# Optimization experiments

Measured on AMD Instinct MI355X. Metric: run time of the kernel, lower is better.

## Reference

```python
import jax, jax.numpy as jnp
import numpy as np
from jax import lax

NPOINT = 2048
NSAMPLE = 32
RADIUS = 0.2


def setup_inputs() -> dict:
    key = jax.random.key(0)
    ks = jax.random.split(key, 6)
    B, N, C = 4, 16384, 64
    xyz = jax.random.normal(ks[0], (B, N, 3), jnp.float32)
    features = jax.random.normal(ks[1], (B, C, N), jnp.float32)

    def w(k, o, i):
        return jax.random.normal(k, (o, i), jnp.float32) * (1.0 / np.sqrt(i))

    W1 = w(ks[2], 64, C + 3)
    b1 = jnp.zeros((64,), jnp.float32)
    W2 = w(ks[3], 64, 64)
    b2 = jnp.zeros((64,), jnp.float32)
    W3 = w(ks[4], 128, 64)
    b3 = jnp.zeros((128,), jnp.float32)
    return {"xyz": xyz, "features": features, "W1": W1, "b1": b1,
            "W2": W2, "b2": b2, "W3": W3, "b3": b3}


def _fps(xyz, npoint):
    # Iterative furthest point sampling. xyz: (B, N, 3) -> (B, npoint) int32.
    B, N, _ = xyz.shape

    def step(carry, _):
        dist, last = carry  # dist: (B, N) running min sq-dist to chosen set
        p = jnp.take_along_axis(xyz, last[:, None, None], axis=1)  # (B,1,3)
        d = jnp.sum((xyz - p) ** 2, axis=-1)                        # (B,N)
        dist = jnp.minimum(dist, d)
        nxt = jnp.argmax(dist, axis=-1).astype(jnp.int32)
        return (dist, nxt), nxt

    init = (jnp.full((B, N), 1e10, xyz.dtype), jnp.zeros((B,), jnp.int32))
    _, rest = lax.scan(step, init, None, length=npoint - 1)  # (npoint-1, B)
    idx = jnp.concatenate([jnp.zeros((1, B), jnp.int32), rest], axis=0)
    return idx.T  # (B, npoint)


def _ball_query(xyz, new_xyz):
    # For each centroid pick up to NSAMPLE points within RADIUS (first-found
    # semantics, matching the PointNet++ CUDA ball_query: pad with first hit).
    B, N, _ = xyz.shape
    d2 = jnp.sum((new_xyz[:, :, None, :] - xyz[:, None, :, :]) ** 2, axis=-1)  # (B,S,N)
    cand = jnp.where(d2 < RADIUS * RADIUS, jnp.arange(N, dtype=jnp.int32), N)
    neg_vals, _ = lax.top_k(-cand, NSAMPLE)  # smallest NSAMPLE indices, in order
    sel = -neg_vals                           # (B,S,NSAMPLE)
    first = sel[..., :1]
    sel = jnp.where(sel == N, first, sel)     # pad empties with first hit
    return jnp.where(sel == N, 0, sel)        # fully-empty balls -> index 0


def reference(xyz, features, W1, b1, W2, b2, W3, b3):
    new_xyz_idx = _fps(xyz, NPOINT)                              # (B, S)
    new_xyz = jnp.take_along_axis(xyz, new_xyz_idx[..., None], axis=1)  # (B,S,3)
    idx = _ball_query(xyz, new_xyz)                              # (B,S,ns)
    B, S, ns = idx.shape
    C = features.shape[1]
    # Gather + center neighbor xyz: (B, 3, S, ns)
    gx = jnp.take_along_axis(xyz, idx.reshape(B, S * ns, 1), axis=1)
    gx = gx.reshape(B, S, ns, 3) - new_xyz[:, :, None, :]
    gx = gx.transpose(0, 3, 1, 2)
    # Gather neighbor features: (B, C, S, ns)
    gf = jnp.take_along_axis(features, idx.reshape(B, 1, S * ns), axis=2)
    gf = gf.reshape(B, C, S, ns)
    x = jnp.concatenate([gx, gf], axis=1)  # (B, C+3, S, ns)
    # SharedMLP: 1x1 conv + ReLU stack
    for W, b in ((W1, b1), (W2, b2), (W3, b3)):
        x = jax.nn.relu(jnp.einsum('oi,bisn->bosn', W, x) + b[None, :, None, None])
    new_features = x.max(axis=-1)  # (B, 128, S)
    return new_xyz, new_xyz_idx, new_features, idx
```

## Files before the change

### kernel.cpp

```cpp
#include <hip/hip_runtime.h>
#include <cstdint>

#define BATCH   4
#define NPTS    16384
#define NCH     64
#define NPOINT  2048
#define NSAMP   32

#define OFF_XYZ  0
#define OFF_IDX1 (BATCH*NPOINT*3)
#define OFF_FEAT (OFF_IDX1 + BATCH*NPOINT)
#define OFF_IDX3 (OFF_FEAT + BATCH*128*NPOINT)


__device__ __forceinline__ float sqd_exact(float dx, float dy, float dz) {
    float a = __fmul_rn(dx, dx);
    float b = __fmul_rn(dy, dy);
    float c = __fmul_rn(dz, dz);
    return __fadd_rn(__fadd_rn(a, b), c);
}

__device__ __forceinline__ int part3(int v) {
    return (v & 1) | ((v & 2) << 2) | ((v & 4) << 4) | ((v & 8) << 6);
}

__device__ __forceinline__ float wave_max_nonneg(float x) {
    int v;
    v = __builtin_amdgcn_update_dpp(0, __float_as_int(x), 0x111, 0xf, 0xf, false);
    x = fmaxf(x, __int_as_float(v));
    v = __builtin_amdgcn_update_dpp(0, __float_as_int(x), 0x112, 0xf, 0xf, false);
    x = fmaxf(x, __int_as_float(v));
    v = __builtin_amdgcn_update_dpp(0, __float_as_int(x), 0x114, 0xf, 0xf, false);
    x = fmaxf(x, __int_as_float(v));
    v = __builtin_amdgcn_update_dpp(0, __float_as_int(x), 0x118, 0xf, 0xf, false);
    x = fmaxf(x, __int_as_float(v));
    v = __builtin_amdgcn_update_dpp(0, __float_as_int(x), 0x142, 0xa, 0xf, false);
    x = fmaxf(x, __int_as_float(v));
    v = __builtin_amdgcn_update_dpp(0, __float_as_int(x), 0x143, 0xc, 0xf, false);
    x = fmaxf(x, __int_as_float(v));
    return __int_as_float(__builtin_amdgcn_readlane(__float_as_int(x), 63));
}

__device__ __forceinline__ unsigned long long wave_max_u64(unsigned hi, unsigned lo) {
#define STAGE(ctrl, rmask)                                                      \
    {                                                                           \
        unsigned ohi = (unsigned)__builtin_amdgcn_update_dpp(0, (int)hi, ctrl, rmask, 0xf, false); \
        unsigned olo = (unsigned)__builtin_amdgcn_update_dpp(0, (int)lo, ctrl, rmask, 0xf, false); \
        bool take = (ohi > hi) || ((ohi == hi) & (olo > lo));                   \
        hi = take ? ohi : hi;                                                   \
        lo = take ? olo : lo;                                                   \
    }
    STAGE(0x111, 0xf)
    STAGE(0x112, 0xf)
    STAGE(0x114, 0xf)
    STAGE(0x118, 0xf)
    STAGE(0x142, 0xa)
    STAGE(0x143, 0xc)
#undef STAGE
    unsigned rhi = (unsigned)__builtin_amdgcn_readlane((int)hi, 63);
    unsigned rlo = (unsigned)__builtin_amdgcn_readlane((int)lo, 63);
    return ((unsigned long long)rhi << 32) | rlo;
}

__global__ __launch_bounds__(1024)
void binsort_kernel(const float* __restrict__ xyz, float* __restrict__ out) {
    const int b = blockIdx.x, t = threadIdx.x, lane = t & 63, wv = t >> 6;
    float* scr  = out + OFF_FEAT;
    float* sx   = scr + (size_t)b * NPTS;
    float* sy   = scr + (size_t)(BATCH + b) * NPTS;
    float* sz   = scr + (size_t)(2 * BATCH + b) * NPTS;
    int*   sidx = (int*)(scr + (size_t)3 * BATCH * NPTS) + (size_t)b * NPTS;
    const float* xb = xyz + (size_t)b * (NPTS * 3);

    __shared__ int hist[4096];
    __shared__ int wsum[16];
    for (int k = t; k < 4096; k += 1024) hist[k] = 0;
    __syncthreads();

    const int base = t << 4;
    float f[48];
    {
        const float4* v4 = (const float4*)(xb + (size_t)base * 3);
#pragma unroll
        for (int q = 0; q < 12; ++q) {
            float4 v = v4[q];
            f[4*q+0] = v.x; f[4*q+1] = v.y; f[4*q+2] = v.z; f[4*q+3] = v.w;
        }
    }
    int cells[16];
    const float sc = 16.0f / 9.0f;
#pragma unroll
    for (int j = 0; j < 16; ++j) {
        int qx = (int)fminf(fmaxf((f[3*j+0] + 4.5f) * sc, 0.0f), 15.0f);
        int qy = (int)fminf(fmaxf((f[3*j+1] + 4.5f) * sc, 0.0f), 15.0f);
        int qz = (int)fminf(fmaxf((f[3*j+2] + 4.5f) * sc, 0.0f), 15.0f);
        cells[j] = part3(qx) | (part3(qy) << 1) | (part3(qz) << 2);
        atomicAdd(&hist[cells[j]], 1);
    }
    __syncthreads();

    int h0 = hist[4*t], h1 = hist[4*t+1], h2 = hist[4*t+2], h3 = hist[4*t+3];
    int s = h0 + h1 + h2 + h3;
    int ps = s;
#pragma unroll
    for (int off = 1; off <= 32; off <<= 1) {
        int o = __shfl_up(ps, off, 64);
        if (lane >= off) ps += o;
    }
    if (lane == 63) wsum[wv] = ps;
    __syncthreads();
    int wbase = 0;
    for (int w = 0; w < wv; ++w) wbase += wsum[w];
    int excl = wbase + ps - s;
    hist[4*t]   = excl;
    hist[4*t+1] = excl + h0;
    hist[4*t+2] = excl + h0 + h1;
    hist[4*t+3] = excl + h0 + h1 + h2;
    __syncthreads();

#pragma unroll
    for (int j = 0; j < 16; ++j) {
        int pos = atomicAdd(&hist[cells[j]], 1);
        sx[pos] = f[3*j+0]; sy[pos] = f[3*j+1]; sz[pos] = f[3*j+2];
        sidx[pos] = base + j;
    }
}

__global__ __launch_bounds__(1024)
void fps_kernel(const float* __restrict__ xyz, float* __restrict__ out) {
    const int b = blockIdx.x, t = threadIdx.x, lane = t & 63, wv = t >> 6;
    const float* scr  = out + OFF_FEAT;
    const float* sxp  = scr + (size_t)b * NPTS;
    const float* syp  = scr + (size_t)(BATCH + b) * NPTS;
    const float* szp  = scr + (size_t)(2 * BATCH + b) * NPTS;
    const int*   sip  = (const int*)(scr + (size_t)3 * BATCH * NPTS) + (size_t)b * NPTS;
    const float* __restrict__ xb = xyz + (size_t)b * (NPTS * 3);
    float* oxyz = out + OFF_XYZ  + (size_t)b * (NPOINT * 3);
    float* oidx = out + OFF_IDX1 + (size_t)b * NPOINT;

    const int base = t << 4;
    float px[16], py[16], pz[16], dist[16];
    unsigned idx2[8];
    {
        const float4* vx = (const float4*)(sxp + base);
        const float4* vy = (const float4*)(syp + base);
        const float4* vz = (const float4*)(szp + base);
        const int4*   vi = (const int4*)(sip + base);
#pragma unroll
        for (int q = 0; q < 4; ++q) {
            float4 a = vx[q]; px[4*q] = a.x; px[4*q+1] = a.y; px[4*q+2] = a.z; px[4*q+3] = a.w;
            float4 c = vy[q]; py[4*q] = c.x; py[4*q+1] = c.y; py[4*q+2] = c.z; py[4*q+3] = c.w;
            float4 d = vz[q]; pz[4*q] = d.x; pz[4*q+1] = d.y; pz[4*q+2] = d.z; pz[4*q+3] = d.w;
            int4   i = vi[q];
            idx2[2*q]   = (unsigned)i.x | ((unsigned)i.y << 16);
            idx2[2*q+1] = (unsigned)i.z | ((unsigned)i.w << 16);
        }
    }
    float bnx = px[0], bxx = px[0], bny = py[0], bxy = py[0], bnz = pz[0], bxz = pz[0];
#pragma unroll
    for (int j = 1; j < 16; ++j) {
        bnx = fminf(bnx, px[j]); bxx = fmaxf(bxx, px[j]);
        bny = fminf(bny, py[j]); bxy = fmaxf(bxy, py[j]);
        bnz = fminf(bnz, pz[j]); bxz = fmaxf(bxz, pz[j]);
    }
#pragma unroll
    for (int j = 0; j < 16; ++j) dist[j] = 1e10f;
    unsigned long long mk = 0;
    float maxdG = 1e10f;

    __shared__ unsigned long long s_k[2][16];

    float cx = xb[0], cy = xb[1], cz = xb[2];
    if (t == 0) { oxyz[0] = cx; oxyz[1] = cy; oxyz[2] = cz; oidx[0] = 0.0f; }

    for (int it = 1; it < NPOINT; ++it) {
        const int q = it & 1;
        float dxl = fmaxf(fmaxf(bnx - cx, cx - bxx), 0.0f);
        float dyl = fmaxf(fmaxf(bny - cy, cy - bxy), 0.0f);
        float dzl = fmaxf(fmaxf(bnz - cz, cz - bxz), 0.0f);
        float bb  = dxl * dxl + dyl * dyl + dzl * dzl;
        if (bb * 0.99999f < maxdG) {
            float mv = 0.0f;
#pragma unroll
            for (int j = 0; j < 16; ++j) {
                float d  = sqd_exact(__fsub_rn(px[j], cx),
                                     __fsub_rn(py[j], cy),
                                     __fsub_rn(pz[j], cz));
                float nd = fminf(dist[j], d);
                dist[j] = nd;
                mv = fmaxf(mv, nd);
            }
            int bi = 0xFFFF;
#pragma unroll
            for (int j = 0; j < 16; ++j) {
                int oi = (int)((idx2[j >> 1] >> ((j & 1) * 16)) & 0xFFFFu);
                if (dist[j] == mv) bi = min(bi, oi);
            }
            mk = ((unsigned long long)__float_as_uint(mv) << 32) | (unsigned)(~bi);
            maxdG = mv;
        }
        float wm = wave_max_nonneg(maxdG);
        bool cand = (maxdG == wm);
        unsigned long long msk = __ballot(cand);
        if (__popcll(msk) > 1) {
            unsigned long long best = 0;
            unsigned long long m2 = msk;
            while (m2) {
                int l = __ffsll(m2) - 1;
                unsigned long long omk = __shfl(mk, l, 64);
                best = best > omk ? best : omk;
                m2 &= m2 - 1;
            }
            cand = cand && (mk == best);
        }
        if (cand) s_k[q][wv] = mk;
        __syncthreads();
        unsigned long long kv = s_k[q][lane & 15];
        unsigned long long gk = wave_max_u64((unsigned)(kv >> 32), (unsigned)kv);
        const int gi = (int)(~(unsigned)gk);
        cx = xb[gi*3+0]; cy = xb[gi*3+1]; cz = xb[gi*3+2];
        if (t == 0) {
            oxyz[it*3+0] = cx; oxyz[it*3+1] = cy; oxyz[it*3+2] = cz;
            oidx[it] = (float)gi;
        }
    }
}

__global__ __launch_bounds__(256)
void ballq_kernel(const float* __restrict__ xyz, float* __restrict__ out) {
    const int b    = blockIdx.y;
    const int t    = threadIdx.x;
    const int lane = t & 63;
    const int wv   = t >> 6;
    const int s    = blockIdx.x * 4 + wv;
    const float* __restrict__ xb = xyz + (size_t)b * (NPTS * 3);

    const float* ctr = out + OFF_XYZ + ((size_t)(b * NPOINT + s)) * 3;
    const float cx = ctr[0], cy = ctr[1], cz = ctr[2];

    __shared__ float sx[256], sy[256], sz[256];
    __shared__ int   lists[4][NSAMP];

    int have = 0;
    for (int tile = 0; tile < NPTS / 256; ++tile) {
        const int pi = tile * 256 + t;
        const float* p = xb + (size_t)pi * 3;
        float ax = p[0], ay = p[1], az = p[2];
        sx[t] = ax; sy[t] = ay; sz[t] = az;
        __syncthreads();
        if (have < NSAMP) {
#pragma unroll
            for (int sub = 0; sub < 4; ++sub) {
                const int li = sub * 64 + lane;
                float d2 = sqd_exact(__fsub_rn(cx, sx[li]),
                                     __fsub_rn(cy, sy[li]),
                                     __fsub_rn(cz, sz[li]));
                bool hit = d2 < 0.04f;
                unsigned long long m = __ballot(hit);
                if (hit) {
                    int pos = have + (int)__popcll(m & ((1ull << lane) - 1ull));
                    if (pos < NSAMP) lists[wv][pos] = tile * 256 + li;
                }
                have += (int)__popcll(m);
                if (have >= NSAMP) break;
            }
        }
        __syncthreads();
    }
    if (lane < NSAMP) {
        int hv = have < NSAMP ? have : NSAMP;
        int v0 = (have > 0) ? lists[wv][0] : 0;
        int v  = (lane < hv) ? lists[wv][lane] : v0;
        out[OFF_IDX3 + ((size_t)(b * NPOINT + s)) * NSAMP + lane] = (float)v;
    }
}

__global__ __launch_bounds__(256)
void mlp_kernel(const float* __restrict__ xyz, const float* __restrict__ feat,
                const float* __restrict__ W1, const float* __restrict__ b1,
                const float* __restrict__ W2, const float* __restrict__ b2,
                const float* __restrict__ W3, const float* __restrict__ b3,
                float* __restrict__ out) {
    const int s = blockIdx.x;
    const int b = blockIdx.y;
    const int t = threadIdx.x;

    __shared__ __align__(16) float Wbuf[64 * 128];
    __shared__ float Xs[67 * 32];
    __shared__ float H1[64 * 32];
    __shared__ float H2[64 * 32];
    __shared__ int   idxs[NSAMP];
    __shared__ float ctr[3];

    if (t < NSAMP) idxs[t] = (int)out[OFF_IDX3 + ((size_t)(b * NPOINT + s)) * NSAMP + t];
    if (t < 3)     ctr[t]  = out[OFF_XYZ + ((size_t)(b * NPOINT + s)) * 3 + t];
    for (int k = t; k < 67 * 64; k += 256) {
        int i = k >> 6, o = k & 63;
        Wbuf[k] = W1[o * 67 + i];
    }
    __syncthreads();

    const float* xb = xyz  + (size_t)b * (NPTS * 3);
    const float* fb = feat + (size_t)b * (NCH * NPTS);
    for (int k = t; k < 67 * 32; k += 256) {
        int i = k >> 5, n = k & 31;
        int ii = idxs[n];
        float v;
        if (i < 3) v = __fsub_rn(xb[(size_t)ii * 3 + i], ctr[i]);
        else       v = fb[(size_t)(i - 3) * NPTS + ii];
        Xs[k] = v;
    }
    __syncthreads();

    const int n  = t & 31;
    const int og = t >> 5;

    {
        const int o0 = og * 8;
        float acc[8] = {0,0,0,0,0,0,0,0};
        for (int i = 0; i < 67; ++i) {
            float x = Xs[i * 32 + n];
            const float4* wp = (const float4*)&Wbuf[i * 64 + o0];
            float4 w0 = wp[0], w1 = wp[1];
            acc[0] += w0.x * x; acc[1] += w0.y * x; acc[2] += w0.z * x; acc[3] += w0.w * x;
            acc[4] += w1.x * x; acc[5] += w1.y * x; acc[6] += w1.z * x; acc[7] += w1.w * x;
        }
#pragma unroll
        for (int k = 0; k < 8; ++k)
            H1[(o0 + k) * 32 + n] = fmaxf(acc[k] + b1[o0 + k], 0.0f);
    }
    __syncthreads();
    for (int k = t; k < 64 * 64; k += 256) {
        int i = k >> 6, o = k & 63;
        Wbuf[k] = W2[o * 64 + i];
    }
    __syncthreads();

    {
        const int o0 = og * 8;
        float acc[8] = {0,0,0,0,0,0,0,0};
        for (int i = 0; i < 64; ++i) {
            float x = H1[i * 32 + n];
            const float4* wp = (const float4*)&Wbuf[i * 64 + o0];
            float4 w0 = wp[0], w1 = wp[1];
            acc[0] += w0.x * x; acc[1] += w0.y * x; acc[2] += w0.z * x; acc[3] += w0.w * x;
            acc[4] += w1.x * x; acc[5] += w1.y * x; acc[6] += w1.z * x; acc[7] += w1.w * x;
        }
#pragma unroll
        for (int k = 0; k < 8; ++k)
            H2[(o0 + k) * 32 + n] = fmaxf(acc[k] + b2[o0 + k], 0.0f);
    }
    __syncthreads();
    for (int k = t; k < 64 * 128; k += 256) {
        int i = k >> 7, o = k & 127;
        Wbuf[k] = W3[o * 64 + i];
    }
    __syncthreads();

    {
        const int o0 = og * 16;
        float acc[16];
#pragma unroll
        for (int k = 0; k < 16; ++k) acc[k] = 0.0f;
        for (int i = 0; i < 64; ++i) {
            float x = H2[i * 32 + n];
            const float4* wp = (const float4*)&Wbuf[i * 128 + o0];
            float4 w0 = wp[0], w1 = wp[1], w2 = wp[2], w3 = wp[3];
            acc[0]  += w0.x * x; acc[1]  += w0.y * x; acc[2]  += w0.z * x; acc[3]  += w0.w * x;
            acc[4]  += w1.x * x; acc[5]  += w1.y * x; acc[6]  += w1.z * x; acc[7]  += w1.w * x;
            acc[8]  += w2.x * x; acc[9]  += w2.y * x; acc[10] += w2.z * x; acc[11] += w2.w * x;
            acc[12] += w3.x * x; acc[13] += w3.y * x; acc[14] += w3.z * x; acc[15] += w3.w * x;
        }
#pragma unroll
        for (int k = 0; k < 16; ++k) {
            float h = fmaxf(acc[k] + b3[o0 + k], 0.0f);
#pragma unroll
            for (int off = 16; off >= 1; off >>= 1)
                h = fmaxf(h, __shfl_xor(h, off, 64));
            if (n == 0)
                out[OFF_FEAT + (size_t)b * 128 * NPOINT + (size_t)(o0 + k) * NPOINT + s] = h;
        }
    }
}

extern "C" void kernel_launch(void* const* d_in, const int* in_sizes, int n_in,
                              void* d_out, int out_size, void* d_ws, size_t ws_size,
                              hipStream_t stream) {
    const float* xyz  = (const float*)d_in[0];
    const float* feat = (const float*)d_in[1];
    const float* W1   = (const float*)d_in[2];
    const float* b1   = (const float*)d_in[3];
    const float* W2   = (const float*)d_in[4];
    const float* b2   = (const float*)d_in[5];
    const float* W3   = (const float*)d_in[6];
    const float* b3   = (const float*)d_in[7];
    float* out = (float*)d_out;

    binsort_kernel<<<BATCH, 1024, 0, stream>>>(xyz, out);
    fps_kernel<<<BATCH, 1024, 0, stream>>>(xyz, out);
    ballq_kernel<<<dim3(NPOINT / 4, BATCH), 256, 0, stream>>>(xyz, out);
    mlp_kernel<<<dim3(NPOINT, BATCH), 256, 0, stream>>>(xyz, feat, W1, b1, W2, b2, W3, b3, out);
}
```

Measured before the change: 3.063 ms.

## Compact active FPS buckets into a worklist and spread updates across threads

Each FPS iteration now builds a shared-memory worklist of spatial buckets whose bounding box could still change, and spreads their point updates over four threads per bucket. Running distances live in LDS rather than registers, and points are stored as packed float4 (xyz plus index) in scratch memory. The aim is to stop idle threads waiting on the few active buckets each iteration. The cost is three barriers per iteration instead of one, plus atomics and LDS and global traffic for every active bucket.

```diff
diff --git a/kernel.cpp b/kernel.cpp
--- a/kernel.cpp
+++ b/kernel.cpp
@@ -6,6 +6,7 @@
 #define NCH     64
 #define NPOINT  2048
 #define NSAMP   32
+#define NBUCK   (NPTS / 16)
 
 #define OFF_XYZ  0
 #define OFF_IDX1 (BATCH*NPOINT*3)
@@ -22,23 +23,6 @@
 
 __device__ __forceinline__ int part3(int v) {
     return (v & 1) | ((v & 2) << 2) | ((v & 4) << 4) | ((v & 8) << 6);
-}
-
-__device__ __forceinline__ float wave_max_nonneg(float x) {
-    int v;
-    v = __builtin_amdgcn_update_dpp(0, __float_as_int(x), 0x111, 0xf, 0xf, false);
-    x = fmaxf(x, __int_as_float(v));
-    v = __builtin_amdgcn_update_dpp(0, __float_as_int(x), 0x112, 0xf, 0xf, false);
-    x = fmaxf(x, __int_as_float(v));
-    v = __builtin_amdgcn_update_dpp(0, __float_as_int(x), 0x114, 0xf, 0xf, false);
-    x = fmaxf(x, __int_as_float(v));
-    v = __builtin_amdgcn_update_dpp(0, __float_as_int(x), 0x118, 0xf, 0xf, false);
-    x = fmaxf(x, __int_as_float(v));
-    v = __builtin_amdgcn_update_dpp(0, __float_as_int(x), 0x142, 0xa, 0xf, false);
-    x = fmaxf(x, __int_as_float(v));
-    v = __builtin_amdgcn_update_dpp(0, __float_as_int(x), 0x143, 0xc, 0xf, false);
-    x = fmaxf(x, __int_as_float(v));
-    return __int_as_float(__builtin_amdgcn_readlane(__float_as_int(x), 63));
 }
 
 __device__ __forceinline__ unsigned long long wave_max_u64(unsigned hi, unsigned lo) {
@@ -65,11 +49,7 @@
 __global__ __launch_bounds__(1024)
 void binsort_kernel(const float* __restrict__ xyz, float* __restrict__ out) {
     const int b = blockIdx.x, t = threadIdx.x, lane = t & 63, wv = t >> 6;
-    float* scr  = out + OFF_FEAT;
-    float* sx   = scr + (size_t)b * NPTS;
-    float* sy   = scr + (size_t)(BATCH + b) * NPTS;
-    float* sz   = scr + (size_t)(2 * BATCH + b) * NPTS;
-    int*   sidx = (int*)(scr + (size_t)3 * BATCH * NPTS) + (size_t)b * NPTS;
+    float4* pts4 = (float4*)(out + OFF_FEAT) + (size_t)b * NPTS;
     const float* xb = xyz + (size_t)b * (NPTS * 3);
 
     __shared__ int hist[4096];
@@ -121,103 +101,115 @@
 #pragma unroll
     for (int j = 0; j < 16; ++j) {
         int pos = atomicAdd(&hist[cells[j]], 1);
-        sx[pos] = f[3*j+0]; sy[pos] = f[3*j+1]; sz[pos] = f[3*j+2];
-        sidx[pos] = base + j;
+        pts4[pos] = make_float4(f[3*j+0], f[3*j+1], f[3*j+2],
+                                __int_as_float(base + j));
     }
 }
 
 __global__ __launch_bounds__(1024)
 void fps_kernel(const float* __restrict__ xyz, float* __restrict__ out) {
-    const int b = blockIdx.x, t = threadIdx.x, lane = t & 63, wv = t >> 6;
-    const float* scr  = out + OFF_FEAT;
-    const float* sxp  = scr + (size_t)b * NPTS;
-    const float* syp  = scr + (size_t)(BATCH + b) * NPTS;
-    const float* szp  = scr + (size_t)(2 * BATCH + b) * NPTS;
-    const int*   sip  = (const int*)(scr + (size_t)3 * BATCH * NPTS) + (size_t)b * NPTS;
+    const int b = blockIdx.x, t = threadIdx.x, lane = t & 63;
+    const float4* __restrict__ pts = (const float4*)(out + OFF_FEAT) + (size_t)b * NPTS;
     const float* __restrict__ xb = xyz + (size_t)b * (NPTS * 3);
     float* oxyz = out + OFF_XYZ  + (size_t)b * (NPOINT * 3);
     float* oidx = out + OFF_IDX1 + (size_t)b * NPOINT;
 
-    const int base = t << 4;
-    float px[16], py[16], pz[16], dist[16];
-    unsigned idx2[8];
-    {
-        const float4* vx = (const float4*)(sxp + base);
-        const float4* vy = (const float4*)(syp + base);
-        const float4* vz = (const float4*)(szp + base);
-        const int4*   vi = (const int4*)(sip + base);
-#pragma unroll
-        for (int q = 0; q < 4; ++q) {
-            float4 a = vx[q]; px[4*q] = a.x; px[4*q+1] = a.y; px[4*q+2] = a.z; px[4*q+3] = a.w;
-            float4 c = vy[q]; py[4*q] = c.x; py[4*q+1] = c.y; py[4*q+2] = c.z; py[4*q+3] = c.w;
-            float4 d = vz[q]; pz[4*q] = d.x; pz[4*q+1] = d.y; pz[4*q+2] = d.z; pz[4*q+3] = d.w;
-            int4   i = vi[q];
-            idx2[2*q]   = (unsigned)i.x | ((unsigned)i.y << 16);
-            idx2[2*q+1] = (unsigned)i.z | ((unsigned)i.w << 16);
-        }
-    }
-    float bnx = px[0], bxx = px[0], bny = py[0], bxy = py[0], bnz = pz[0], bxz = pz[0];
-#pragma unroll
-    for (int j = 1; j < 16; ++j) {
-        bnx = fminf(bnx, px[j]); bxx = fmaxf(bxx, px[j]);
-        bny = fminf(bny, py[j]); bxy = fmaxf(bxy, py[j]);
-        bnz = fminf(bnz, pz[j]); bxz = fmaxf(bxz, pz[j]);
-    }
-#pragma unroll
-    for (int j = 0; j < 16; ++j) dist[j] = 1e10f;
-    unsigned long long mk = 0;
+    __shared__ float s_dist[NPTS];
+    __shared__ unsigned long long s_key[NBUCK];
+    __shared__ int s_wl[NBUCK];
+    __shared__ int s_cnt;
+    __shared__ unsigned long long s_gkey;
+
+    float bnx, bxx, bny, bxy, bnz, bxz;
+    {
+        float4 p0 = pts[t * 16];
+        bnx = bxx = p0.x; bny = bxy = p0.y; bnz = bxz = p0.z;
+#pragma unroll
+        for (int j = 1; j < 16; ++j) {
+            float4 p = pts[t * 16 + j];
+            bnx = fminf(bnx, p.x); bxx = fmaxf(bxx, p.x);
+            bny = fminf(bny, p.y); bxy = fmaxf(bxy, p.y);
+            bnz = fminf(bnz, p.z); bxz = fmaxf(bxz, p.z);
+        }
+        float4 big = make_float4(1e10f, 1e10f, 1e10f, 1e10f);
+#pragma unroll
+        for (int k = 0; k < 4; ++k)
+            *(float4*)&s_dist[t * 16 + k * 4] = big;
+    }
     float maxdG = 1e10f;
-
-    __shared__ unsigned long long s_k[2][16];
+    unsigned long long kv = 0;
+    if (t == 0) { s_cnt = 0; s_gkey = 0ull; }
 
     float cx = xb[0], cy = xb[1], cz = xb[2];
     if (t == 0) { oxyz[0] = cx; oxyz[1] = cy; oxyz[2] = cz; oidx[0] = 0.0f; }
+    __syncthreads();
 
     for (int it = 1; it < NPOINT; ++it) {
-        const int q = it & 1;
         float dxl = fmaxf(fmaxf(bnx - cx, cx - bxx), 0.0f);
         float dyl = fmaxf(fmaxf(bny - cy, cy - bxy), 0.0f);
         float dzl = fmaxf(fmaxf(bnz - cz, cz - bxz), 0.0f);
         float bb  = dxl * dxl + dyl * dyl + dzl * dzl;
-        if (bb * 0.99999f < maxdG) {
-            float mv = 0.0f;
-#pragma unroll
-            for (int j = 0; j < 16; ++j) {
-                float d  = sqd_exact(__fsub_rn(px[j], cx),
-                                     __fsub_rn(py[j], cy),
-                                     __fsub_rn(pz[j], cz));
-                float nd = fminf(dist[j], d);
-                dist[j] = nd;
-                mv = fmaxf(mv, nd);
+        bool active = (bb * 0.99999f < maxdG);
+        unsigned long long m = __ballot(active);
+        int cntw = (int)__popcll(m);
+        if (cntw) {
+            int basep = 0;
+            if (lane == 0) basep = atomicAdd(&s_cnt, cntw);
+            basep = __shfl(basep, 0, 64);
+            if (active) {
+                int pos = basep + (int)__popcll(m & ((1ull << lane) - 1ull));
+                s_wl[pos] = t;
             }
-            int bi = 0xFFFF;
-#pragma unroll
-            for (int j = 0; j < 16; ++j) {
-                int oi = (int)((idx2[j >> 1] >> ((j & 1) * 16)) & 0xFFFFu);
-                if (dist[j] == mv) bi = min(bi, oi);
+        }
+        __syncthreads();
+        if (t == 0) s_gkey = 0ull;
+        const int K = s_cnt;
+        const int sub = t & 3;
+        for (int w = t >> 2; w < K; w += 256) {
+            const int bid = s_wl[w];
+            const int p0  = bid * 16 + sub * 4;
+            float4 P0 = pts[p0 + 0], P1 = pts[p0 + 1],
+                   P2 = pts[p0 + 2], P3 = pts[p0 + 3];
+            float4 dv = *(float4*)&s_dist[p0];
+            float mv = -1.0f; int bi = 0x7FFFFFFF;
+#define UPD(P, DD)                                                              \
+            {                                                                   \
+                float d  = sqd_exact(__fsub_rn(P.x, cx),                        \
+                                     __fsub_rn(P.y, cy),                        \
+                                     __fsub_rn(P.z, cz));                       \
+                float nd = fminf(DD, d);                                        \
+                DD = nd;                                                        \
+                int oi = __float_as_int(P.w);                                   \
+                bool bet = (nd > mv) || ((nd == mv) & (oi < bi));               \
+                mv = bet ? nd : mv;                                             \
+                bi = bet ? oi : bi;                                             \
             }
-            mk = ((unsigned long long)__float_as_uint(mv) << 32) | (unsigned)(~bi);
-            maxdG = mv;
-        }
-        float wm = wave_max_nonneg(maxdG);
-        bool cand = (maxdG == wm);
-        unsigned long long msk = __ballot(cand);
-        if (__popcll(msk) > 1) {
-            unsigned long long best = 0;
-            unsigned long long m2 = msk;
-            while (m2) {
-                int l = __ffsll(m2) - 1;
-                unsigned long long omk = __shfl(mk, l, 64);
-                best = best > omk ? best : omk;
-                m2 &= m2 - 1;
+            UPD(P0, dv.x) UPD(P1, dv.y) UPD(P2, dv.z) UPD(P3, dv.w)
+#undef UPD
+            *(float4*)&s_dist[p0] = dv;
+#pragma unroll
+            for (int off = 1; off <= 2; off <<= 1) {
+                float omv = __shfl_xor(mv, off, 64);
+                int   obi = __shfl_xor(bi, off, 64);
+                bool take = (omv > mv) || ((omv == mv) & (obi < bi));
+                mv = take ? omv : mv;
+                bi = take ? obi : bi;
             }
-            cand = cand && (mk == best);
-        }
-        if (cand) s_k[q][wv] = mk;
-        __syncthreads();
-        unsigned long long kv = s_k[q][lane & 15];
-        unsigned long long gk = wave_max_u64((unsigned)(kv >> 32), (unsigned)kv);
-        const int gi = (int)(~(unsigned)gk);
+            if (sub == 0)
+                s_key[bid] = ((unsigned long long)__float_as_uint(mv) << 32)
+                           | (unsigned)((~bi) & 0xFFFF);
+        }
+        __syncthreads();
+        if (active) {
+            kv = s_key[t];
+            maxdG = __uint_as_float((unsigned)(kv >> 32));
+        }
+        unsigned long long wk = wave_max_u64((unsigned)(kv >> 32), (unsigned)kv);
+        if (lane == 0) atomicMax(&s_gkey, wk);
+        if (t == 0) s_cnt = 0;
+        __syncthreads();
+        unsigned long long gk = s_gkey;
+        const int gi = (int)((~(unsigned)gk) & 0xFFFFu);
         cx = xb[gi*3+0]; cy = xb[gi*3+1]; cz = xb[gi*3+2];
         if (t == 0) {
             oxyz[it*3+0] = cx; oxyz[it*3+1] = cy; oxyz[it*3+2] = cz;
```

Result: slower. 3.778 ms (+23.3%).
